# Performance work log

Measured on AMD Instinct MI355X. Metric: run time of the kernel, lower is better.

The kernel has to match this reference:

```python
import jax, jax.numpy as jnp
import numpy as np

HEAD_DIM = 64
N_HEADS = 16
D_MODEL = 2048
SEQ = 2048
BATCH = 1
LAYER_IDX = 12
LN_EPS = 1e-5


def setup_inputs() -> dict:
    key = jax.random.key(0)
    ks = jax.random.split(key, 8)
    s = 0.02
    return {
        "x": jax.random.normal(ks[0], (BATCH, SEQ, D_MODEL), dtype=jnp.float32),
        "W_qkv": jax.random.normal(ks[1], (3 * N_HEADS * 2 * HEAD_DIM, D_MODEL), dtype=jnp.float32) * s,
        "W_o": jax.random.normal(ks[2], (D_MODEL, D_MODEL), dtype=jnp.float32) * s,
        "lambda_q1": jax.random.normal(ks[3], (2 * HEAD_DIM,), dtype=jnp.float32) * 0.1,
        "lambda_k1": jax.random.normal(ks[4], (2 * HEAD_DIM,), dtype=jnp.float32) * 0.1,
        "lambda_q2": jax.random.normal(ks[5], (2 * HEAD_DIM,), dtype=jnp.float32) * 0.1,
        "lambda_k2": jax.random.normal(ks[6], (2 * HEAD_DIM,), dtype=jnp.float32) * 0.1,
        "gn_gamma": jnp.ones((N_HEADS, 2 * HEAD_DIM), dtype=jnp.float32),
        "gn_beta": jnp.zeros((N_HEADS, 2 * HEAD_DIM), dtype=jnp.float32),
    }


def _causal_sdpa(q, k, v, scale):
    # q,k: [B,H,S,d], v: [B,H,S,2d]
    S = q.shape[2]
    scores = jnp.einsum("bhqd,bhkd->bhqk", q, k) * scale
    causal = jnp.tril(jnp.ones((S, S), dtype=bool))
    scores = jnp.where(causal[None, None], scores, jnp.float32(-1e30))
    attn = jax.nn.softmax(scores, axis=-1)
    return jnp.einsum("bhqk,bhkd->bhqd", attn, v)


def reference(x, W_qkv, W_o, lambda_q1, lambda_k1, lambda_q2, lambda_k2, gn_gamma, gn_beta):
    B, S, D = x.shape
    lambda_init = 0.8 - 0.6 * jnp.exp(jnp.float32(-0.3 * LAYER_IDX))
    scale = HEAD_DIM ** -0.5

    qkv = x @ W_qkv.T  # [B,S,6*H*d]
    qkv = qkv.reshape(B, S, 3, N_HEADS, 2 * HEAD_DIM)
    q = jnp.transpose(qkv[:, :, 0], (0, 2, 1, 3))  # [B,H,S,2d]
    k = jnp.transpose(qkv[:, :, 1], (0, 2, 1, 3))
    v = jnp.transpose(qkv[:, :, 2], (0, 2, 1, 3))
    q1, q2 = q[..., :HEAD_DIM], q[..., HEAD_DIM:]
    k1, k2 = k[..., :HEAD_DIM], k[..., HEAD_DIM:]

    lam = jnp.exp(lambda_q1 * lambda_k1) - jnp.exp(lambda_q2 * lambda_k2) + lambda_init  # [2d]

    A1 = _causal_sdpa(q1, k1, v, scale)
    A2 = _causal_sdpa(q2, k2, v, scale)
    out = A1 - lam * A2  # broadcast over value channel [B,H,S,2d]

    # per-head LayerNorm over last dim
    mu = jnp.mean(out, axis=-1, keepdims=True)
    var = jnp.mean((out - mu) ** 2, axis=-1, keepdims=True)
    out = (out - mu) * jax.lax.rsqrt(var + LN_EPS)
    out = out * gn_gamma[None, :, None, :] + gn_beta[None, :, None, :]

    out = out * (1.0 - lambda_init)
    out = jnp.transpose(out, (0, 2, 1, 3)).reshape(B, S, D)
    return out @ W_o.T
```

## Files before the change

kernel.cpp:

```cpp
#include <hip/hip_runtime.h>

typedef short short8 __attribute__((ext_vector_type(8)));
typedef float f32x4 __attribute__((ext_vector_type(4)));
typedef unsigned short u16;
typedef u16 u16x8 __attribute__((ext_vector_type(8)));
typedef u16 u16x4 __attribute__((ext_vector_type(4)));

#define AS1 __attribute__((address_space(1)))
#define AS3 __attribute__((address_space(3)))

__device__ static inline void load16_lds(const void* g, void* l) {
    __builtin_amdgcn_global_load_lds((AS1 void*)g, (AS3 void*)l, 16, 0, 0);
}

__device__ static inline u16 f2bf(float f) {
    union { float f; unsigned u; } v; v.f = f;
    unsigned r = v.u + 0x7fffu + ((v.u >> 16) & 1u);
    return (u16)(r >> 16);
}

__global__ __launch_bounds__(256) void cast_kernel(const float* __restrict__ in,
                                                   u16* __restrict__ out, int n) {
    int i = (blockIdx.x * 256 + threadIdx.x) * 4;
    if (i + 3 < n) {
        f32x4 v = *(const f32x4*)&in[i];
        u16x4 o;
        o[0] = f2bf(v[0]); o[1] = f2bf(v[1]); o[2] = f2bf(v[2]); o[3] = f2bf(v[3]);
        *(u16x4*)&out[i] = o;
    }
}

template <int MODE>
__global__ __launch_bounds__(256) void gemm_bt(const u16* __restrict__ A,
                                               const u16* __restrict__ B,
                                               int M, int N, int K,
                                               float* __restrict__ C,
                                               u16* __restrict__ Qo,
                                               u16* __restrict__ Ko,
                                               u16* __restrict__ Vo) {
    __shared__ u16 As[128 * 32];
    __shared__ u16 Bs[128 * 32];
    const int tid  = threadIdx.x;
    const int lane = tid & 63, wave = tid >> 6;
    const int quad = lane >> 4, l15 = lane & 15;
    const int wm = wave >> 1, wn = wave & 1;
    const int m0 = blockIdx.y * 128;
    const int n0 = blockIdx.x * 128;

    f32x4 acc[4][4] = {};

    const int ar = tid >> 2, ac = tid & 3;
    for (int k0 = 0; k0 < K; k0 += 32) {
        __syncthreads();
        load16_lds(&A[(m0 + ar) * K + k0 + ac * 8],      &As[tid * 8]);
        load16_lds(&A[(m0 + ar + 64) * K + k0 + ac * 8], &As[(tid + 256) * 8]);
        load16_lds(&B[(n0 + ar) * K + k0 + ac * 8],      &Bs[tid * 8]);
        load16_lds(&B[(n0 + ar + 64) * K + k0 + ac * 8], &Bs[(tid + 256) * 8]);
        __syncthreads();
        short8 af[4], bf[4];
#pragma unroll
        for (int mt = 0; mt < 4; mt++)
            af[mt] = *(const short8*)&As[(wm * 64 + mt * 16 + l15) * 32 + quad * 8];
#pragma unroll
        for (int nt = 0; nt < 4; nt++)
            bf[nt] = *(const short8*)&Bs[(wn * 64 + nt * 16 + l15) * 32 + quad * 8];
#pragma unroll
        for (int mt = 0; mt < 4; mt++)
#pragma unroll
            for (int nt = 0; nt < 4; nt++)
                acc[mt][nt] = __builtin_amdgcn_mfma_f32_16x16x32_bf16(af[mt], bf[nt], acc[mt][nt], 0, 0, 0);
    }

#pragma unroll
    for (int mt = 0; mt < 4; mt++) {
#pragma unroll
        for (int nt = 0; nt < 4; nt++) {
#pragma unroll
            for (int r = 0; r < 4; r++) {
                int row = m0 + wm * 64 + mt * 16 + quad * 4 + r;
                int col = n0 + wn * 64 + nt * 16 + l15;
                float v = acc[mt][nt][r];
                if (MODE == 0) {
                    C[(long)row * N + col] = v;
                } else {
                    int comp = col >> 11, h = (col >> 7) & 15, d = col & 127;
                    u16 bv = f2bf(comp == 0 ? v * 0.18033688f : v);
                    u16* dst = (comp == 0) ? Qo : ((comp == 1) ? Ko : Vo);
                    dst[((h * 2048) + row) * 128 + d] = bv;
                }
            }
        }
    }
}

__global__ __launch_bounds__(256) void transpose_v(const u16* __restrict__ vb,
                                                   u16* __restrict__ vT) {
    __shared__ u16 T[64 * 136];
    const int s0 = blockIdx.x * 64, h = blockIdx.y;
    const int tid = threadIdx.x;
#pragma unroll
    for (int i = 0; i < 4; i++) {
        int c = tid + i * 256;
        int s = c >> 4, dch = c & 15;
        *(u16x8*)&T[s * 136 + dch * 8] =
            *(const u16x8*)&vb[((h * 2048) + s0 + s) * 128 + dch * 8];
    }
    __syncthreads();
#pragma unroll
    for (int i = 0; i < 4; i++) {
        int c = tid + i * 256;
        int d = c >> 3, sch = c & 7;
        u16x8 o;
#pragma unroll
        for (int j = 0; j < 8; j++) o[j] = T[(sch * 8 + j) * 136 + d];
        *(u16x8*)&vT[((h * 128) + d) * 2048 + s0 + sch * 8] = o;
    }
}

__global__ __launch_bounds__(256, 4) void attn_kernel(const u16* __restrict__ qb,
                                                      const u16* __restrict__ kb,
                                                      const u16* __restrict__ vT,
                                                      float* __restrict__ ob) {
    const int bid = blockIdx.x;
    const int h = bid & 15;
    const int comp = (bid >> 4) & 1;
    const int j = bid >> 5;
    const int qt = (j < 16) ? (2 * j + 1) : (62 - 2 * j);
    const int tid = threadIdx.x, lane = tid & 63, wave = tid >> 6;
    const int quad = lane >> 4, l15 = lane & 15;

    __shared__ u16 Ks[64 * 64];
    __shared__ u16 VsT[128 * 64];
    __shared__ u16 Ps[4][16 * 72];

    const u16* kb_h = &kb[(size_t)h * 2048 * 128 + comp * 64];
    const u16* vT_h = &vT[(size_t)h * 128 * 2048];

    const int c1 = tid, c2 = tid + 256;
    const int k1key = c1 >> 3, k1dc = ((c1 & 7) ^ k1key) & 7;
    const int k2key = c2 >> 3, k2dc = ((c2 & 7) ^ k2key) & 7;
    const u16* kaddr1 = &kb_h[k1key * 128 + k1dc * 8];
    const u16* kaddr2 = &kb_h[k2key * 128 + k2dc * 8];
    const u16* vaddr[4];
#pragma unroll
    for (int i = 0; i < 4; i++) {
        int c = tid + i * 256;
        int dim = c >> 3, kc = ((c & 7) ^ dim) & 7;
        vaddr[i] = &vT_h[dim * 2048 + kc * 8];
    }

    const int qrow = qt * 64 + wave * 16 + l15;
    short8 aq[2];
#pragma unroll
    for (int ks = 0; ks < 2; ks++)
        aq[ks] = *(const short8*)&qb[((h * 2048) + qrow) * 128 + comp * 64 + ks * 32 + quad * 8];

    float l_acc[4] = {0.f, 0.f, 0.f, 0.f};
    f32x4 o[8] = {};

    u16x8 kst0, kst1, vst[4];

    kst0 = *(const u16x8*)(kaddr1);
    kst1 = *(const u16x8*)(kaddr2);
#pragma unroll
    for (int i = 0; i < 4; i++) vst[i] = *(const u16x8*)(vaddr[i]);

    for (int kt = 0; kt <= qt; kt++) {
        *(u16x8*)&Ks[c1 * 8] = kst0;
        *(u16x8*)&Ks[c2 * 8] = kst1;
#pragma unroll
        for (int i = 0; i < 4; i++) *(u16x8*)&VsT[(tid + i * 256) * 8] = vst[i];
        __syncthreads();

        if (kt < qt) {
            const int nkt = kt + 1;
            kst0 = *(const u16x8*)(kaddr1 + nkt * 8192);
            kst1 = *(const u16x8*)(kaddr2 + nkt * 8192);
#pragma unroll
            for (int i = 0; i < 4; i++) vst[i] = *(const u16x8*)(vaddr[i] + nkt * 64);
        }

        f32x4 s[4];
#pragma unroll
        for (int kn = 0; kn < 4; kn++) {
            f32x4 a = {};
#pragma unroll
            for (int ks = 0; ks < 2; ks++) {
                int key = kn * 16 + l15;
                int dc = ks * 4 + quad;
                short8 b = *(const short8*)&Ks[(key * 8 + ((dc ^ key) & 7)) * 8];
                a = __builtin_amdgcn_mfma_f32_16x16x32_bf16(aq[ks], b, a, 0, 0, 0);
            }
            s[kn] = a;
        }
        if (kt == qt) {
#pragma unroll
            for (int kn = 0; kn < 4; kn++)
#pragma unroll
                for (int r = 0; r < 4; r++) {
                    int ql = wave * 16 + quad * 4 + r, kl = kn * 16 + l15;
                    if (kl > ql) s[kn][r] = -1e30f;
                }
        }

        u16* pw = &Ps[wave][0];
#pragma unroll
        for (int kn = 0; kn < 4; kn++)
#pragma unroll
            for (int r = 0; r < 4; r++) {
                float p = exp2f(s[kn][r]);
                l_acc[r] += p;
                pw[(quad * 4 + r) * 72 + kn * 16 + l15] = f2bf(p);
            }
        asm volatile("s_waitcnt lgkmcnt(0)\n" ::: "memory");

#pragma unroll
        for (int ks2 = 0; ks2 < 2; ks2++) {
            short8 pa = *(const short8*)&pw[l15 * 72 + ks2 * 32 + quad * 8];
#pragma unroll
            for (int nt = 0; nt < 8; nt++) {
                int dim = nt * 16 + l15;
                int kc = ks2 * 4 + quad;
                short8 bv = *(const short8*)&VsT[(dim * 8 + ((kc ^ dim) & 7)) * 8];
                o[nt] = __builtin_amdgcn_mfma_f32_16x16x32_bf16(pa, bv, o[nt], 0, 0, 0);
            }
        }
        __syncthreads();
    }

#pragma unroll
    for (int off = 1; off < 16; off <<= 1)
#pragma unroll
        for (int r = 0; r < 4; r++) l_acc[r] += __shfl_xor(l_acc[r], off);
    float rl[4];
#pragma unroll
    for (int r = 0; r < 4; r++) rl[r] = 1.f / l_acc[r];

    const int srow = qt * 64 + wave * 16 + quad * 4;
#pragma unroll
    for (int nt = 0; nt < 8; nt++)
#pragma unroll
        for (int r = 0; r < 4; r++) {
            float v = o[nt][r] * rl[r];
            ob[(((comp * 16 + h) * 2048) + srow + r) * 128 + nt * 16 + l15] = v;
        }
}

__global__ __launch_bounds__(256) void combine_kernel(const float* __restrict__ ob,
                                                      const float* __restrict__ lq1,
                                                      const float* __restrict__ lk1,
                                                      const float* __restrict__ lq2,
                                                      const float* __restrict__ lk2,
                                                      const float* __restrict__ gamma,
                                                      const float* __restrict__ beta,
                                                      u16* __restrict__ attn) {
    const int tid = threadIdx.x, wave = tid >> 6, lane = tid & 63;
    const int row = blockIdx.x * 4 + wave;
    const int s = row >> 4, h = row & 15;
    const float lambda_init = 0.8f - 0.6f * __expf(-3.6f);
    const int d0 = lane * 2;
    float vals[2];
#pragma unroll
    for (int j = 0; j < 2; j++) {
        int d = d0 + j;
        float a1 = ob[((h)*2048 + s) * 128 + d];
        float a2 = ob[((16 + h) * 2048 + s) * 128 + d];
        float lam = __expf(lq1[d] * lk1[d]) - __expf(lq2[d] * lk2[d]) + lambda_init;
        vals[j] = a1 - lam * a2;
    }
    float sum = vals[0] + vals[1];
    float sq = vals[0] * vals[0] + vals[1] * vals[1];
#pragma unroll
    for (int off = 1; off < 64; off <<= 1) {
        sum += __shfl_xor(sum, off);
        sq += __shfl_xor(sq, off);
    }
    float mu = sum * (1.f / 128.f);
    float var = sq * (1.f / 128.f) - mu * mu;
    float rinv = rsqrtf(var + 1e-5f);
    float osc = 1.f - lambda_init;
#pragma unroll
    for (int j = 0; j < 2; j++) {
        int d = d0 + j;
        float g = gamma[h * 128 + d], b = beta[h * 128 + d];
        float v = ((vals[j] - mu) * rinv * g + b) * osc;
        attn[s * 2048 + h * 128 + d] = f2bf(v);
    }
}

extern "C" void kernel_launch(void* const* d_in, const int* in_sizes, int n_in,
                              void* d_out, int out_size, void* d_ws, size_t ws_size,
                              hipStream_t stream) {
    (void)in_sizes; (void)n_in; (void)out_size; (void)ws_size;
    const float* x    = (const float*)d_in[0];
    const float* Wqkv = (const float*)d_in[1];
    const float* Wo   = (const float*)d_in[2];
    const float* lq1  = (const float*)d_in[3];
    const float* lk1  = (const float*)d_in[4];
    const float* lq2  = (const float*)d_in[5];
    const float* lk2  = (const float*)d_in[6];
    const float* gam  = (const float*)d_in[7];
    const float* bet  = (const float*)d_in[8];
    float* out = (float*)d_out;

    char* ws = (char*)d_ws;
    u16*   xb    = (u16*)(ws);
    u16*   wqkvb = (u16*)(ws + (size_t)(8 << 20));
    float* ob    = (float*)(ws + (size_t)(8 << 20));
    u16*   wob   = (u16*)(ws + (size_t)(40 << 20));
    u16*   qb    = (u16*)(ws + (size_t)(48 << 20));
    u16*   kb    = (u16*)(ws + (size_t)(56 << 20));
    u16*   vb    = (u16*)(ws + (size_t)(64 << 20));
    u16*   vT    = (u16*)(ws + (size_t)(72 << 20));
    u16*   attn  = (u16*)(ws);

    cast_kernel<<<(2048 * 2048) / 1024, 256, 0, stream>>>(x, xb, 2048 * 2048);
    cast_kernel<<<(6144 * 2048) / 1024, 256, 0, stream>>>(Wqkv, wqkvb, 6144 * 2048);
    cast_kernel<<<(2048 * 2048) / 1024, 256, 0, stream>>>(Wo, wob, 2048 * 2048);
    gemm_bt<1><<<dim3(48, 16), 256, 0, stream>>>(xb, wqkvb, 2048, 6144, 2048,
                                                 nullptr, qb, kb, vb);
    transpose_v<<<dim3(32, 16), 256, 0, stream>>>(vb, vT);
    attn_kernel<<<1024, 256, 0, stream>>>(qb, kb, vT, ob);
    combine_kernel<<<8192, 256, 0, stream>>>(ob, lq1, lk1, lq2, lk2, gam, bet, attn);
    gemm_bt<0><<<dim3(16, 16), 256, 0, stream>>>(attn, wob, 2048, 2048, 2048,
                                                 out, nullptr, nullptr, nullptr);
}
```

Before: 318.9 us.

## Register-prefetch GEMM tiles with swizzled LDS and templated tile sizes

Replaces the direct global-to-LDS loads in the bf16 GEMM with register-staged prefetch of the next K slice, overlapping global latency with MFMA work on the current tile. LDS is now XOR-swizzled to cut bank conflicts on fragment reads. The kernel is templated on BM/BN and min-waves, and the output projection switches to a 128x64 tile, doubling its grid to 512 blocks to fill more CUs. The QKV epilogue hoists the per-column comp/head decode to once per block. Costs are more registers for the staged tiles and an extra register-to-LDS write pass per iteration.

```diff
diff --git a/kernel.cpp b/kernel.cpp
--- a/kernel.cpp
+++ b/kernel.cpp
@@ -5,13 +5,6 @@
 typedef unsigned short u16;
 typedef u16 u16x8 __attribute__((ext_vector_type(8)));
 typedef u16 u16x4 __attribute__((ext_vector_type(4)));
-
-#define AS1 __attribute__((address_space(1)))
-#define AS3 __attribute__((address_space(3)))
-
-__device__ static inline void load16_lds(const void* g, void* l) {
-    __builtin_amdgcn_global_load_lds((AS1 void*)g, (AS3 void*)l, 16, 0, 0);
-}
 
 __device__ static inline u16 f2bf(float f) {
     union { float f; unsigned u; } v; v.f = f;
@@ -30,66 +23,108 @@
     }
 }
 
-template <int MODE>
-__global__ __launch_bounds__(256) void gemm_bt(const u16* __restrict__ A,
-                                               const u16* __restrict__ B,
-                                               int M, int N, int K,
-                                               float* __restrict__ C,
-                                               u16* __restrict__ Qo,
-                                               u16* __restrict__ Ko,
-                                               u16* __restrict__ Vo) {
-    __shared__ u16 As[128 * 32];
-    __shared__ u16 Bs[128 * 32];
+template <int BM, int BN, int MODE, int MINW>
+__global__ __launch_bounds__(256, MINW) void gemm_bt(const u16* __restrict__ A,
+                                                     const u16* __restrict__ B,
+                                                     int M, int N, int K,
+                                                     float* __restrict__ C,
+                                                     u16* __restrict__ Qo,
+                                                     u16* __restrict__ Ko,
+                                                     u16* __restrict__ Vo) {
+    constexpr int APT = BM * 4 / 256;
+    constexpr int BPT = BN * 4 / 256;
+    constexpr int MT = BM / 32, NT = BN / 32;
+    __shared__ u16 As[BM * 32];
+    __shared__ u16 Bs[BN * 32];
     const int tid  = threadIdx.x;
     const int lane = tid & 63, wave = tid >> 6;
     const int quad = lane >> 4, l15 = lane & 15;
     const int wm = wave >> 1, wn = wave & 1;
-    const int m0 = blockIdx.y * 128;
-    const int n0 = blockIdx.x * 128;
-
-    f32x4 acc[4][4] = {};
-
-    const int ar = tid >> 2, ac = tid & 3;
+    const int m0 = blockIdx.y * BM;
+    const int n0 = blockIdx.x * BN;
+
+    f32x4 acc[MT][NT] = {};
+
+    const u16* aga[APT];
+    const u16* bga[BPT];
+#pragma unroll
+    for (int i = 0; i < APT; i++) {
+        int s = tid + i * 256, r = s >> 2;
+        int kg = (s & 3) ^ ((r >> 1) & 3);
+        aga[i] = &A[(size_t)(m0 + r) * K + kg * 8];
+    }
+#pragma unroll
+    for (int i = 0; i < BPT; i++) {
+        int s = tid + i * 256, r = s >> 2;
+        int kg = (s & 3) ^ ((r >> 1) & 3);
+        bga[i] = &B[(size_t)(n0 + r) * K + kg * 8];
+    }
+
+    u16x8 ast[APT], bst[BPT];
+#pragma unroll
+    for (int i = 0; i < APT; i++) ast[i] = *(const u16x8*)aga[i];
+#pragma unroll
+    for (int i = 0; i < BPT; i++) bst[i] = *(const u16x8*)bga[i];
+
     for (int k0 = 0; k0 < K; k0 += 32) {
+        if (k0) __syncthreads();
+#pragma unroll
+        for (int i = 0; i < APT; i++) *(u16x8*)&As[(tid + i * 256) * 8] = ast[i];
+#pragma unroll
+        for (int i = 0; i < BPT; i++) *(u16x8*)&Bs[(tid + i * 256) * 8] = bst[i];
         __syncthreads();
-        load16_lds(&A[(m0 + ar) * K + k0 + ac * 8],      &As[tid * 8]);
-        load16_lds(&A[(m0 + ar + 64) * K + k0 + ac * 8], &As[(tid + 256) * 8]);
-        load16_lds(&B[(n0 + ar) * K + k0 + ac * 8],      &Bs[tid * 8]);
-        load16_lds(&B[(n0 + ar + 64) * K + k0 + ac * 8], &Bs[(tid + 256) * 8]);
-        __syncthreads();
-        short8 af[4], bf[4];
-#pragma unroll
-        for (int mt = 0; mt < 4; mt++)
-            af[mt] = *(const short8*)&As[(wm * 64 + mt * 16 + l15) * 32 + quad * 8];
-#pragma unroll
-        for (int nt = 0; nt < 4; nt++)
-            bf[nt] = *(const short8*)&Bs[(wn * 64 + nt * 16 + l15) * 32 + quad * 8];
-#pragma unroll
-        for (int mt = 0; mt < 4; mt++)
-#pragma unroll
-            for (int nt = 0; nt < 4; nt++)
+        if (k0 + 32 < K) {
+#pragma unroll
+            for (int i = 0; i < APT; i++) ast[i] = *(const u16x8*)(aga[i] + k0 + 32);
+#pragma unroll
+            for (int i = 0; i < BPT; i++) bst[i] = *(const u16x8*)(bga[i] + k0 + 32);
+        }
+
+        short8 af[MT], bf[NT];
+#pragma unroll
+        for (int mt = 0; mt < MT; mt++) {
+            int row = wm * (BM / 2) + mt * 16 + l15;
+            int slot = row * 4 + (quad ^ ((row >> 1) & 3));
+            af[mt] = *(const short8*)&As[slot * 8];
+        }
+#pragma unroll
+        for (int nt = 0; nt < NT; nt++) {
+            int row = wn * (BN / 2) + nt * 16 + l15;
+            int slot = row * 4 + (quad ^ ((row >> 1) & 3));
+            bf[nt] = *(const short8*)&Bs[slot * 8];
+        }
+#pragma unroll
+        for (int mt = 0; mt < MT; mt++)
+#pragma unroll
+            for (int nt = 0; nt < NT; nt++)
                 acc[mt][nt] = __builtin_amdgcn_mfma_f32_16x16x32_bf16(af[mt], bf[nt], acc[mt][nt], 0, 0, 0);
     }
 
-#pragma unroll
-    for (int mt = 0; mt < 4; mt++) {
-#pragma unroll
-        for (int nt = 0; nt < 4; nt++) {
-#pragma unroll
-            for (int r = 0; r < 4; r++) {
-                int row = m0 + wm * 64 + mt * 16 + quad * 4 + r;
-                int col = n0 + wn * 64 + nt * 16 + l15;
-                float v = acc[mt][nt][r];
-                if (MODE == 0) {
-                    C[(long)row * N + col] = v;
-                } else {
-                    int comp = col >> 11, h = (col >> 7) & 15, d = col & 127;
-                    u16 bv = f2bf(comp == 0 ? v * 0.18033688f : v);
-                    u16* dst = (comp == 0) ? Qo : ((comp == 1) ? Ko : Vo);
-                    dst[((h * 2048) + row) * 128 + d] = bv;
+    if (MODE == 0) {
+#pragma unroll
+        for (int mt = 0; mt < MT; mt++)
+#pragma unroll
+            for (int nt = 0; nt < NT; nt++)
+#pragma unroll
+                for (int r = 0; r < 4; r++) {
+                    int row = m0 + wm * (BM / 2) + mt * 16 + quad * 4 + r;
+                    int col = n0 + wn * (BN / 2) + nt * 16 + l15;
+                    C[(size_t)row * N + col] = acc[mt][nt][r];
                 }
-            }
-        }
+    } else {
+        const int comp = n0 >> 11, h = (n0 >> 7) & 15;
+        u16* dst = (comp == 0) ? Qo : ((comp == 1) ? Ko : Vo);
+        const float sc = (comp == 0) ? 0.18033688f : 1.0f;
+#pragma unroll
+        for (int mt = 0; mt < MT; mt++)
+#pragma unroll
+            for (int nt = 0; nt < NT; nt++)
+#pragma unroll
+                for (int r = 0; r < 4; r++) {
+                    int row = m0 + wm * (BM / 2) + mt * 16 + quad * 4 + r;
+                    int d = wn * (BN / 2) + nt * 16 + l15;
+                    dst[((h * 2048) + row) * 128 + d] = f2bf(acc[mt][nt][r] * sc);
+                }
     }
 }
 
@@ -159,7 +194,6 @@
     f32x4 o[8] = {};
 
     u16x8 kst0, kst1, vst[4];
-
     kst0 = *(const u16x8*)(kaddr1);
     kst1 = *(const u16x8*)(kaddr2);
 #pragma unroll
@@ -317,11 +351,11 @@
     cast_kernel<<<(2048 * 2048) / 1024, 256, 0, stream>>>(x, xb, 2048 * 2048);
     cast_kernel<<<(6144 * 2048) / 1024, 256, 0, stream>>>(Wqkv, wqkvb, 6144 * 2048);
     cast_kernel<<<(2048 * 2048) / 1024, 256, 0, stream>>>(Wo, wob, 2048 * 2048);
-    gemm_bt<1><<<dim3(48, 16), 256, 0, stream>>>(xb, wqkvb, 2048, 6144, 2048,
-                                                 nullptr, qb, kb, vb);
+    gemm_bt<128, 128, 1, 3><<<dim3(48, 16), 256, 0, stream>>>(
+        xb, wqkvb, 2048, 6144, 2048, nullptr, qb, kb, vb);
     transpose_v<<<dim3(32, 16), 256, 0, stream>>>(vb, vT);
     attn_kernel<<<1024, 256, 0, stream>>>(qb, kb, vT, ob);
     combine_kernel<<<8192, 256, 0, stream>>>(ob, lq1, lk1, lq2, lk2, gam, bet, attn);
-    gemm_bt<0><<<dim3(16, 16), 256, 0, stream>>>(attn, wob, 2048, 2048, 2048,
-                                                 out, nullptr, nullptr, nullptr);
-}
+    gemm_bt<128, 64, 0, 2><<<dim3(32, 16), 256, 0, stream>>>(
+        attn, wob, 2048, 2048, 2048, out, nullptr, nullptr, nullptr);
+}
```

Result: faster. 298.6 us (-6.4%).
